# Kernel optimization log

Hardware: AMD Instinct MI355X
Metric: run time of the kernel (lower is better)

Reference implementation:

```python
import jax, jax.numpy as jnp
import numpy as np

NC = 2            # num_classes
CONF_THR = 0.7
IOU_THR = 0.2

_PI, _PJ = np.triu_indices(9, k=1)   # 36 candidate edge directions for min-area rect


def _decode_level(out, stride):
    # out: [C,h,w]; scale (x,y) channels by stride and add the pixel grid, flatten to [h*w, C]
    C, h, w = out.shape
    gw = (stride * jnp.arange(w, dtype=out.dtype))[None, :]
    gh = (stride * jnp.arange(h, dtype=out.dtype))[:, None]
    out = out.at[NC + 1].set(out[NC + 1] * stride + gw)
    out = out.at[NC + 2].set(out[NC + 2] * stride + gh)
    return out.reshape(C, -1).T


def _min_area_polygons(pts18):
    # pts18: (N,18) interleaved (a,b) coordinate pairs of 9 points.
    # Min-area enclosing rectangle: optimal rect is aligned with some point-pair direction;
    # brute-force all 36 pairs (superset of hull edges) -> exact result, fully vectorized.
    P = pts18.reshape(-1, 9, 2)                       # (N,9,2)
    d = P[:, _PJ] - P[:, _PI]                         # (N,36,2)
    nrm = jnp.sqrt(jnp.sum(d * d, -1) + 1e-12)
    c, s = d[..., 0] / nrm, d[..., 1] / nrm           # (N,36)
    a, b = P[..., 0][:, None, :], P[..., 1][:, None, :]   # (N,1,9)
    u = a * c[..., None] + b * s[..., None]           # rotate by -theta
    v = -a * s[..., None] + b * c[..., None]
    umin, umax = u.min(-1), u.max(-1)
    vmin, vmax = v.min(-1), v.max(-1)
    area = (umax - umin) * (vmax - vmin)              # (N,36)
    k = jnp.argmin(area, 1)[:, None]
    tk = lambda z: jnp.take_along_axis(z, k, 1)[:, 0]
    c, s, umin, umax, vmin, vmax = map(tk, (c, s, umin, umax, vmin, vmax))
    cu = jnp.stack([umin, umax, umax, umin], -1)      # rect corners in rotated frame
    cv = jnp.stack([vmin, vmin, vmax, vmax], -1)
    ca = cu * c[:, None] - cv * s[:, None]            # rotate back
    cb = cu * s[:, None] + cv * c[:, None]
    return jnp.stack([ca, cb], -1).reshape(-1, 8)     # (N,8) interleaved corners


def _points_in_quad(pts, quad):
    # pts (M,2), quad (4,2) convex with consistent winding -> (M,) bool
    e = jnp.roll(quad, -1, 0) - quad
    r = pts[:, None, :] - quad[None]
    cr = e[None, :, 0] * r[..., 1] - e[None, :, 1] * r[..., 0]
    return (cr >= 0).all(-1) | (cr <= 0).all(-1)


def _box_decoder(rect):
    # rect (N,8) -> (N,5) [cx, cy, w, h, angle]; y_first=True convention from the source
    w = jnp.sqrt((rect[:, 0] - rect[:, 2]) ** 2 + (rect[:, 1] - rect[:, 3]) ** 2)
    h = jnp.sqrt((rect[:, 4] - rect[:, 2]) ** 2 + (rect[:, 5] - rect[:, 3]) ** 2)
    cx = rect[:, 1:8:2].sum(1) * 0.25
    cy = rect[:, 0:8:2].sum(1) * 0.25
    ang = jnp.arctan((rect[:, 0] - rect[:, 2]) / (rect[:, 1] - rect[:, 3]))
    return jnp.stack([cx, cy, w, h, ang], -1)


def _rbox_corners(b):
    cx, cy, w, h, a = b[0], b[1], b[2], b[3], b[4]
    cs, sn = jnp.cos(a), jnp.sin(a)
    lx = jnp.array([-0.5, 0.5, 0.5, -0.5]) * w
    ly = jnp.array([-0.5, -0.5, 0.5, 0.5]) * h
    return jnp.stack([cx + lx * cs - ly * sn, cy + lx * sn + ly * cs], -1)  # (4,2)


def _quad_inter_area(A, B):
    # exact intersection area of two convex quads A,B (4,2):
    # candidates = corners of each inside the other + all 16 edge-edge intersections,
    # sorted by angle around their centroid, masked shoelace.
    inA = _points_in_quad(B, A)
    inB = _points_in_quad(A, B)
    rA = jnp.roll(A, -1, 0) - A
    rB = jnp.roll(B, -1, 0) - B
    qp = B[None] - A[:, None]                                  # (4,4,2)
    den = rA[:, None, 0] * rB[None, :, 1] - rA[:, None, 1] * rB[None, :, 0]
    dsafe = jnp.where(jnp.abs(den) < 1e-9, 1e-9, den)
    t = (qp[..., 0] * rB[None, :, 1] - qp[..., 1] * rB[None, :, 0]) / dsafe
    uu = (qp[..., 0] * rA[:, None, 1] - qp[..., 1] * rA[:, None, 0]) / dsafe
    okx = (jnp.abs(den) > 1e-9) & (t >= 0) & (t <= 1) & (uu >= 0) & (uu <= 1)
    X = A[:, None] + t[..., None] * rA[:, None]
    pts = jnp.concatenate([A, B, X.reshape(16, 2)], 0)          # (24,2)
    val = jnp.concatenate([inB, inA, okx.reshape(16)], 0)
    n = val.sum()
    cen = jnp.sum(jnp.where(val[:, None], pts, 0.0), 0) / jnp.maximum(n, 1)
    rel = pts - cen
    ang = jnp.where(val, jnp.arctan2(rel[:, 1], rel[:, 0]), 1e9)
    o = jnp.argsort(ang)
    rp, vs = rel[o], val[o]
    rp = jnp.where(vs[:, None], rp, rp[0])   # invalid slots -> first valid vertex (zero-area edges)
    nx = jnp.roll(rp, -1, 0)
    area = 0.5 * jnp.abs(jnp.sum(rp[:, 0] * nx[:, 1] - rp[:, 1] * nx[:, 0]))
    return jnp.where(n >= 3, area, 0.0)


def _forward(out3, out4, out5, off1_l3, off1_l4, off1_l5, offf_l3, offf_l4, offf_l5):
    outs = jnp.concatenate([_decode_level(out3[0], 4),
                            _decode_level(out4[0], 8),
                            _decode_level(out5[0], 16)], 0)          # (N, NC+3)
    flat = lambda z: z[0].reshape(18, -1).T
    off1 = jnp.concatenate([flat(off1_l3), flat(off1_l4), flat(off1_l5)], 0)
    offf = jnp.concatenate([flat(offf_l3), flat(offf_l4), flat(offf_l5)], 0) + off1
    N = outs.shape[0]
    x, y = outs[:, NC + 1], outs[:, NC + 2]
    offf = offf + jnp.tile(jnp.stack([y, x], -1), (1, 9))            # (y,x) interleaved, 9 points
    xs, ys = offf[:, 1:18:2], offf[:, 0:18:2]
    area = (xs.max(1) - xs.min(1)) * (ys.max(1) - ys.min(1)) / 40.0
    conf = outs[:, 0]
    conf_mask = conf > CONF_THR * jax.nn.sigmoid(area)
    rect = _min_area_polygons(offf)                                  # (N,8)
    boxes5 = _box_decoder(rect)                                      # (N,5)
    corners = jax.vmap(_rbox_corners)(boxes5)                        # (N,4,2)
    areas5 = boxes5[:, 2] * boxes5[:, 3]
    position = outs[:, NC + 1:]                                      # (N,2) = (x,y)
    pts_yx = jnp.stack([position[:, 1], position[:, 0]], -1)         # (y,x), matches rect plane
    quads = rect.reshape(N, 4, 2)
    order = jnp.argsort(jnp.where(conf_mask, conf, -jnp.inf))[::-1]

    def step(carry, i):
        suppressed, keep = carry
        active = jnp.logical_not(suppressed[i])
        keep = keep.at[i].set(active)
        inside = _points_in_quad(pts_yx, quads[i])                   # points_in_polygons
        inter = jax.vmap(lambda C: _quad_inter_area(corners[i], C))(corners)
        iou = inter / (areas5[i] + areas5 - inter + 1e-9)            # box_iou_rotated
        suppressed = suppressed | (active & (inside | (iou >= IOU_THR)))
        return (suppressed, keep), None

    init = (jnp.logical_not(conf_mask), jnp.zeros(N, dtype=bool))
    (_, keep), _ = jax.lax.scan(step, init, order)

    cls = outs[:, 1:NC + 1]
    maxc = cls.max(1)
    masks = jnp.stack([keep & (cls[:, i] == maxc) for i in range(NC)], 0)  # (NC,N)
    cnt = masks.sum(1)
    result = jnp.where(masks[:, :, None], position[None], 0.0)             # (NC,N,2) padded
    rect_out = rect * keep[:, None].astype(rect.dtype)                     # (N,8) padded
    return cnt, result, rect_out


def setup_inputs() -> dict:
    key = jax.random.key(0)
    shapes = [("out3", (1, NC + 3, 32, 32)), ("out4", (1, NC + 3, 16, 16)), ("out5", (1, NC + 3, 8, 8)),
              ("off1_l3", (1, 18, 32, 32)), ("off1_l4", (1, 18, 16, 16)), ("off1_l5", (1, 18, 8, 8)),
              ("offf_l3", (1, 18, 32, 32)), ("offf_l4", (1, 18, 16, 16)), ("offf_l5", (1, 18, 8, 8))]
    ks = jax.random.split(key, len(shapes))
    return {n: jax.random.normal(k, s, dtype=jnp.float32) for (n, s), k in zip(shapes, ks)}


def reference(out3, out4, out5, off1_l3, off1_l4, off1_l5, offf_l3, offf_l4, offf_l5):
    return _forward(out3, out4, out5, off1_l3, off1_l4, off1_l5, offf_l3, offf_l4, offf_l5)
```

## Files before the change

kernel.cpp:

```cpp
#include <hip/hip_runtime.h>
#include <math.h>

#define N_DET 1344
#define MW_MAX 8
#define T2S 9
#define QCAP 2048


__device__ __forceinline__ bool pt_in_quad4(const float* qx, const float* qy,
                                            float px, float py) {
    bool allp = true, alln = true;
#pragma unroll
    for (int k = 0; k < 4; k++) {
        int k1 = (k + 1) & 3;
        float ex = qx[k1] - qx[k], ey = qy[k1] - qy[k];
        float rx = px - qx[k],     ry = py - qy[k];
        float cr = ex * ry - ey * rx;
        allp = allp && (cr >= 0.f);
        alln = alln && (cr <= 0.f);
    }
    return allp || alln;
}

__device__ float quad_inter_area(const float* Ax, const float* Ay,
                                 const float* Bx, const float* By) {
    float px[24], py[24];
    unsigned vmask = 0;
    int n = 0;
#pragma unroll
    for (int k = 0; k < 4; k++) {
        px[k] = Ax[k]; py[k] = Ay[k];
        if (pt_in_quad4(Bx, By, Ax[k], Ay[k])) { vmask |= 1u << k; n++; }
    }
#pragma unroll
    for (int k = 0; k < 4; k++) {
        px[4 + k] = Bx[k]; py[4 + k] = By[k];
        if (pt_in_quad4(Ax, Ay, Bx[k], By[k])) { vmask |= 1u << (4 + k); n++; }
    }
#pragma unroll
    for (int k = 0; k < 4; k++) {
        int k1 = (k + 1) & 3;
        float rax = Ax[k1] - Ax[k], ray = Ay[k1] - Ay[k];
#pragma unroll
        for (int l = 0; l < 4; l++) {
            int l1 = (l + 1) & 3;
            float rbx = Bx[l1] - Bx[l], rby = By[l1] - By[l];
            float qpx = Bx[l] - Ax[k],  qpy = By[l] - Ay[k];
            float den = rax * rby - ray * rbx;
            float ad  = fabsf(den);
            float dsafe = (ad < 1e-9f) ? 1e-9f : den;
            float t = (qpx * rby - qpy * rbx) / dsafe;
            float u = (qpx * ray - qpy * rax) / dsafe;
            bool ok = (ad > 1e-9f) && t >= 0.f && t <= 1.f && u >= 0.f && u <= 1.f;
            int id = 8 + k * 4 + l;
            px[id] = Ax[k] + t * rax;
            py[id] = Ay[k] + t * ray;
            if (ok) { vmask |= 1u << id; n++; }
        }
    }
    float cx = 0.f, cy = 0.f;
#pragma unroll
    for (int m = 0; m < 24; m++)
        if ((vmask >> m) & 1u) { cx += px[m]; cy += py[m]; }
    int mx = (n < 1) ? 1 : n;
    cx = cx / (float)mx;
    cy = cy / (float)mx;

    unsigned long long key[32];
    float sx[32], sy[32];
#pragma unroll
    for (int m = 0; m < 24; m++) {
        float rx = px[m] - cx, ry = py[m] - cy;
        float a = ((vmask >> m) & 1u) ? atan2f(ry, rx) : 1e9f;
        unsigned u = __float_as_uint(a);
        u = (u & 0x80000000u) ? ~u : (u | 0x80000000u);
        key[m] = (((unsigned long long)u) << 6) | (unsigned)m;
        sx[m] = rx; sy[m] = ry;
    }
#pragma unroll
    for (int m = 24; m < 32; m++) { key[m] = ~0ull; sx[m] = 0.f; sy[m] = 0.f; }

#pragma unroll
    for (int k = 2; k <= 32; k <<= 1) {
#pragma unroll
        for (int j = k >> 1; j > 0; j >>= 1) {
#pragma unroll
            for (int t = 0; t < 32; t++) {
                int l = t ^ j;
                if (l > t) {
                    bool up = ((t & k) == 0);
                    bool sw = up ? (key[t] > key[l]) : (key[t] < key[l]);
                    if (sw) {
                        unsigned long long tk = key[t]; key[t] = key[l]; key[l] = tk;
                        float tx = sx[t]; sx[t] = sx[l]; sx[l] = tx;
                        float ty = sy[t]; sy[t] = sy[l]; sy[l] = ty;
                    }
                }
            }
        }
    }

    unsigned ut = __float_as_uint(1e9f) | 0x80000000u;
    unsigned long long kt = ((unsigned long long)ut) << 6;
    float fx = sx[0], fy = sy[0];
    float qx2[24], qy2[24];
#pragma unroll
    for (int m = 0; m < 24; m++) {
        bool v = key[m] < kt;
        qx2[m] = v ? sx[m] : fx;
        qy2[m] = v ? sy[m] : fy;
    }
    float ssum = 0.f;
#pragma unroll
    for (int m = 0; m < 24; m++) {
        int m1 = (m + 1) % 24;
        ssum += qx2[m] * qy2[m1] - qy2[m] * qx2[m1];
    }
    float area = 0.5f * fabsf(ssum);
    return (n >= 3) ? area : 0.f;
}

__device__ bool iou_suppress_c(const float* __restrict__ co_cor,
                               const float* __restrict__ co_a5, int p, int q) {
    float Axr[4], Ayr[4], Bxr[4], Byr[4];
#pragma unroll
    for (int k = 0; k < 4; k++) {
        Axr[k] = co_cor[p * 8 + 2 * k]; Ayr[k] = co_cor[p * 8 + 2 * k + 1];
        Bxr[k] = co_cor[q * 8 + 2 * k]; Byr[k] = co_cor[q * 8 + 2 * k + 1];
    }
    float inter = quad_inter_area(Axr, Ayr, Bxr, Byr);
    float iou = inter / (co_a5[p] + co_a5[q] - inter + 1e-9f);
    return iou >= 0.2f;
}

__global__ void k_decode(const float* __restrict__ out3, const float* __restrict__ out4,
                         const float* __restrict__ out5,
                         const float* __restrict__ o1l3, const float* __restrict__ o1l4,
                         const float* __restrict__ o1l5,
                         const float* __restrict__ ofl3, const float* __restrict__ ofl4,
                         const float* __restrict__ ofl5,
                         float* keyArr, float* cls0, float* cls1, float* xx, float* yy,
                         float* a5, float* ccx, float* ccy, float* rr,
                         float* rect, float* cor, int* Mcnt) {
    int n = blockIdx.x * blockDim.x + threadIdx.x;
    if (n >= N_DET) return;
    if (n == 0) *Mcnt = 0;
    const float *out, *o1, *of;
    int w, idx; float stride;
    if (n < 1024)      { out = out3; o1 = o1l3; of = ofl3; w = 32; idx = n;        stride = 4.f; }
    else if (n < 1280) { out = out4; o1 = o1l4; of = ofl4; w = 16; idx = n - 1024; stride = 8.f; }
    else               { out = out5; o1 = o1l5; of = ofl5; w = 8;  idx = n - 1280; stride = 16.f; }
    int hw = w * w;
    int row = idx / w, col = idx % w;
    float cf = out[0 * hw + idx];
    float c0 = out[1 * hw + idx];
    float c1 = out[2 * hw + idx];
    float x  = out[3 * hw + idx] * stride + stride * (float)col;
    float y  = out[4 * hw + idx] * stride + stride * (float)row;

    float Pa[9], Pb[9];
    float minb = INFINITY, maxb = -INFINITY, mina = INFINITY, maxa = -INFINITY;
#pragma unroll
    for (int k = 0; k < 9; k++) {
        float a = of[(2 * k) * hw + idx]     + o1[(2 * k) * hw + idx]     + y;
        float b = of[(2 * k + 1) * hw + idx] + o1[(2 * k + 1) * hw + idx] + x;
        Pa[k] = a; Pb[k] = b;
        mina = fminf(mina, a); maxa = fmaxf(maxa, a);
        minb = fminf(minb, b); maxb = fmaxf(maxb, b);
    }
    float area = (maxb - minb) * (maxa - mina) / 40.0f;
    float sg = 1.0f / (1.0f + expf(-area));
    int m = (cf > 0.7f * sg) ? 1 : 0;

    float best = INFINITY, bc = 0.f, bs = 0.f;
    float bumin = 0.f, bumax = 0.f, bvmin = 0.f, bvmax = 0.f;
#pragma unroll
    for (int i = 0; i < 9; i++) {
#pragma unroll
        for (int j = i + 1; j < 9; j++) {
            float d0 = Pa[j] - Pa[i], d1 = Pb[j] - Pb[i];
            float nr = sqrtf(d0 * d0 + d1 * d1 + 1e-12f);
            float c = d0 / nr, s = d1 / nr;
            float umin = INFINITY, umax = -INFINITY, vmin = INFINITY, vmax = -INFINITY;
#pragma unroll
            for (int k = 0; k < 9; k++) {
                float u =  Pa[k] * c + Pb[k] * s;
                float v = -Pa[k] * s + Pb[k] * c;
                umin = fminf(umin, u); umax = fmaxf(umax, u);
                vmin = fminf(vmin, v); vmax = fmaxf(vmax, v);
            }
            float ar = (umax - umin) * (vmax - vmin);
            if (ar < best) { best = ar; bc = c; bs = s;
                             bumin = umin; bumax = umax; bvmin = vmin; bvmax = vmax; }
        }
    }
    float cu[4] = {bumin, bumax, bumax, bumin};
    float cv[4] = {bvmin, bvmin, bvmax, bvmax};
    float r8[8];
#pragma unroll
    for (int k = 0; k < 4; k++) {
        r8[2 * k]     = cu[k] * bc - cv[k] * bs;
        r8[2 * k + 1] = cu[k] * bs + cv[k] * bc;
    }
    float w5 = sqrtf((r8[0] - r8[2]) * (r8[0] - r8[2]) + (r8[1] - r8[3]) * (r8[1] - r8[3]));
    float h5 = sqrtf((r8[4] - r8[2]) * (r8[4] - r8[2]) + (r8[5] - r8[3]) * (r8[5] - r8[3]));
    float cx = (r8[1] + r8[3] + r8[5] + r8[7]) * 0.25f;
    float cy = (r8[0] + r8[2] + r8[4] + r8[6]) * 0.25f;
    float ang = atanf((r8[0] - r8[2]) / (r8[1] - r8[3]));
    float cs = cosf(ang), sn = sinf(ang);
    const float lxs[4] = {-0.5f, 0.5f, 0.5f, -0.5f};
    const float lys[4] = {-0.5f, -0.5f, 0.5f, 0.5f};
#pragma unroll
    for (int k = 0; k < 4; k++) {
        cor[n * 8 + 2 * k]     = cx + lxs[k] * w5 * cs - lys[k] * h5 * sn;
        cor[n * 8 + 2 * k + 1] = cy + lxs[k] * w5 * sn + lys[k] * h5 * cs;
    }
#pragma unroll
    for (int k = 0; k < 8; k++) rect[n * 8 + k] = r8[k];
    keyArr[n] = m ? cf : -INFINITY;
    cls0[n] = c0; cls1[n] = c1;
    xx[n] = x; yy[n] = y; a5[n] = w5 * h5;
    ccx[n] = cx; ccy[n] = cy;
    rr[n] = 0.5f * sqrtf(w5 * w5 + h5 * h5);
}

__global__ __launch_bounds__(64) void k_order(
        const float* __restrict__ keyArr,
        const float* __restrict__ xx, const float* __restrict__ yy,
        const float* __restrict__ a5, const float* __restrict__ ccx,
        const float* __restrict__ ccy, const float* __restrict__ rr,
        const float* __restrict__ rect, const float* __restrict__ cor,
        int* order, int* Mcnt,
        float* co_ccx, float* co_ccy, float* co_rr, float* co_a5,
        float* co_xx, float* co_yy, float* co_rect, float* co_cor) {
    int b = blockIdx.x;
    int lane = threadIdx.x;
    float ki = keyArr[b];
    int rank = 0;
    for (int j = lane; j < N_DET; j += 64) {
        float kj = keyArr[j];
        rank += ((kj > ki) || (kj == ki && j > b)) ? 1 : 0;
    }
    for (int off = 32; off; off >>= 1) rank += __shfl_down(rank, off, 64);
    rank = __shfl(rank, 0, 64);
    if (lane == 0) {
        order[rank] = b;
        if (ki != -INFINITY) atomicAdd(Mcnt, 1);
    }
    if (lane < 8)            co_cor[rank * 8 + lane]        = cor[b * 8 + lane];
    else if (lane < 16)      co_rect[rank * 8 + (lane - 8)] = rect[b * 8 + (lane - 8)];
    else if (lane == 16)     co_ccx[rank] = ccx[b];
    else if (lane == 17)     co_ccy[rank] = ccy[b];
    else if (lane == 18)     co_rr[rank]  = rr[b];
    else if (lane == 19)     co_a5[rank]  = a5[b];
    else if (lane == 20)     co_xx[rank]  = xx[b];
    else if (lane == 21)     co_yy[rank]  = yy[b];
}

__global__ __launch_bounds__(256) void k_pairs(
        const float* __restrict__ co_rect, const float* __restrict__ co_cor,
        const float* __restrict__ co_a5,
        const float* __restrict__ co_xx, const float* __restrict__ co_yy,
        const float* __restrict__ co_ccx, const float* __restrict__ co_ccy,
        const float* __restrict__ co_rr,
        const int* __restrict__ Mcnt, unsigned long long* __restrict__ S2) {
    __shared__ unsigned int queue[QCAP];
    __shared__ int qn;
    int M = *Mcnt;
    int MW = (M + 63) >> 6;
    bool fast = (MW <= MW_MAX);
    int tid = threadIdx.x;
    int lane = tid & 63;
    if (tid == 0) qn = 0;
    __syncthreads();

    if (M > 0) {
        int gwave = (blockIdx.x * 256 + tid) >> 6;
        int nwave = (gridDim.x * 256) >> 6;
        int total = M * MW;
        for (int t = gwave; t < total; t += nwave) {
            int p = t / MW;
            int w = t - p * MW;
            int q = w * 64 + lane;
            bool valid = q < M;
            int qc = valid ? q : 0;

            float cbi = co_ccx[p], cai = co_ccy[p], ri = co_rr[p];
            float pjy = co_yy[qc], pjx = co_xx[qc];
            float da = pjy - cai, db = pjx - cbi;
            float rin = ri + 0.1f;
            bool inside = false;
            if (da * da + db * db <= rin * rin) {
                float qxr[4], qyr[4];
#pragma unroll
                for (int k = 0; k < 4; k++) { qxr[k] = co_rect[p * 8 + 2 * k]; qyr[k] = co_rect[p * 8 + 2 * k + 1]; }
                inside = pt_in_quad4(qxr, qyr, pjy, pjx);
            }
            bool bit = valid && inside;
            unsigned long long bb = __ballot(bit);

            float ex = cbi - co_ccx[qc], ey = cai - co_ccy[qc];
            float rs = ri + co_rr[qc] + 0.1f;
            bool needy = valid && (q != p) && !bit && (ex * ex + ey * ey <= rs * rs);

            if (fast) {
                if (lane == 0) S2[p * MW + w] = bb;
                unsigned long long pm = __ballot(needy);
                if (pm) {
                    int cw = __popcll(pm);
                    int base = 0;
                    if (lane == 0) base = atomicAdd(&qn, cw);
                    base = __shfl(base, 0, 64);
                    if (needy) {
                        int pos = base + __popcll(pm & ((1ull << lane) - 1ull));
                        if (pos < QCAP) {
                            queue[pos] = ((unsigned)p << 11) | (unsigned)q;
                        } else {
                            __threadfence();
                            if (iou_suppress_c(co_cor, co_a5, p, q))
                                atomicOr(&S2[p * MW + w], 1ull << (q & 63));
                        }
                    }
                }
            } else {
                bool supp = needy && iou_suppress_c(co_cor, co_a5, p, q);
                unsigned long long sb = __ballot(supp);
                if (lane == 0) S2[p * MW + w] = bb | sb;
            }
        }
    }
    __syncthreads();

    if (M > 0 && fast) {
        int cnt = qn; if (cnt > QCAP) cnt = QCAP;
        for (int t = tid; t < cnt; t += 256) {
            unsigned v = queue[t];
            int p = (int)(v >> 11), q = (int)(v & 2047u);
            if (iou_suppress_c(co_cor, co_a5, p, q))
                atomicOr(&S2[p * MW + (q >> 6)], 1ull << (q & 63));
        }
    }
}

__global__ __launch_bounds__(512) void k_scan_out(
    const float* __restrict__ cls0, const float* __restrict__ cls1,
    const float* __restrict__ xx, const float* __restrict__ yy,
    const float* __restrict__ rect,
    const int* __restrict__ order, const int* __restrict__ Mcnt,
    const unsigned long long* __restrict__ S2, float* __restrict__ out) {
    __shared__ unsigned long long T2[512 * T2S];
    __shared__ unsigned long long Kfin[MW_MAX];
    __shared__ unsigned int keep32[(N_DET + 31) / 32];
    __shared__ int cnt_s[2];
    int tid = threadIdx.x;
    int lane = tid & 63, wid = tid >> 6;
    int M = *Mcnt;
    int MW = (M + 63) >> 6;
    for (int t = tid; t < (N_DET + 31) / 32; t += 512) keep32[t] = 0u;
    if (tid < 2) cnt_s[tid] = 0;
    if (tid < MW_MAX) Kfin[tid] = 0ull;
    __syncthreads();

    if (M > 0 && MW <= MW_MAX) {
        for (int blk = wid; blk < MW * MW; blk += 8) {
            int wp = blk / MW, wq = blk - wp * MW;
            int pp = wp * 64 + lane;
            unsigned long long x = (pp < M) ? S2[pp * MW + wq] : 0ull;
#pragma unroll
            for (int b = 0; b < 64; b++) {
                unsigned long long bb = __ballot((x >> b) & 1ull);
                if (lane == b) T2[(wq * 64 + b) * T2S + wp] = bb;
            }
        }
        __syncthreads();

        if (wid == 0) {
            unsigned long long kw[MW_MAX];
#pragma unroll
            for (int w = 0; w < MW_MAX; w++) {
                int lo = w * 64;
                kw[w] = (M > lo) ? ((M - lo >= 64) ? ~0ull : ((1ull << (M - lo)) - 1ull)) : 0ull;
            }
            unsigned long long pmask = lane ? ((1ull << lane) - 1ull) : 0ull;
            for (int it = 0; it <= M; ++it) {
                bool changed = false;
#pragma unroll
                for (int k = 0; k < MW_MAX; k++) {
                    if (k < MW) {
                        int q = k * 64 + lane;
                        const unsigned long long* row = &T2[q * T2S];
                        unsigned long long sup = 0ull;
#pragma unroll
                        for (int w = 0; w < MW_MAX; w++) {
                            if (w < k)       sup |= row[w] & kw[w];
                            else if (w == k) sup |= row[w] & kw[w] & pmask;
                        }
                        bool nb = (q < M) && (sup == 0ull);
                        unsigned long long nw = __ballot(nb);
                        changed |= (nw != kw[k]);
                        kw[k] = nw;
                    }
                }
                if (!changed) break;
            }
            if (lane == 0) {
#pragma unroll
                for (int w = 0; w < MW_MAX; w++) Kfin[w] = kw[w];
            }
        }
        __syncthreads();
        for (int t = tid; t < M; t += 512) {
            if ((Kfin[t >> 6] >> (t & 63)) & 1ull) {
                int i = order[t];
                atomicOr(&keep32[i >> 5], 1u << (i & 31));
            }
        }
    } else if (M > 0) {
        if (wid == 0) {
            unsigned long long rem = 0ull;
            int lo = lane * 64;
            if (M > lo) rem = (M - lo >= 64) ? ~0ull : ((1ull << (M - lo)) - 1ull);
            for (int guard = 0; guard < N_DET; guard++) {
                unsigned long long vote = __ballot(rem != 0ull);
                if (!vote) break;
                int w = __builtin_ctzll(vote);
                unsigned long long wd = __shfl(rem, w, 64);
                int b = __builtin_ctzll(wd);
                int p = w * 64 + b;
                int i = order[p];
                if (lane == 0) atomicOr(&keep32[i >> 5], 1u << (i & 31));
                unsigned long long rowv = (lane < MW) ? S2[p * MW + lane] : 0ull;
                rem &= ~rowv;
                if (lane == w) rem &= ~(1ull << b);
            }
        }
    }
    __syncthreads();

    int c0 = 0, c1 = 0;
    for (int n = tid; n < N_DET; n += 512) {
        bool kp = (keep32[n >> 5] >> (n & 31)) & 1u;
        float a = cls0[n], b = cls1[n];
        float mxc = fmaxf(a, b);
        bool m0 = kp && (a == mxc);
        bool m1 = kp && (b == mxc);
        float x = xx[n], y = yy[n];
        out[2 + 0 * N_DET * 2 + n * 2 + 0] = m0 ? x : 0.f;
        out[2 + 0 * N_DET * 2 + n * 2 + 1] = m0 ? y : 0.f;
        out[2 + 1 * N_DET * 2 + n * 2 + 0] = m1 ? x : 0.f;
        out[2 + 1 * N_DET * 2 + n * 2 + 1] = m1 ? y : 0.f;
        float kf = kp ? 1.f : 0.f;
#pragma unroll
        for (int k = 0; k < 8; k++)
            out[2 + 2 * N_DET * 2 + n * 8 + k] = rect[n * 8 + k] * kf;
        c0 += m0 ? 1 : 0;
        c1 += m1 ? 1 : 0;
    }
    if (c0) atomicAdd(&cnt_s[0], c0);
    if (c1) atomicAdd(&cnt_s[1], c1);
    __syncthreads();
    if (tid == 0) { out[0] = (float)cnt_s[0]; out[1] = (float)cnt_s[1]; }
}

extern "C" void kernel_launch(void* const* d_in, const int* in_sizes, int n_in,
                              void* d_out, int out_size, void* d_ws, size_t ws_size,
                              hipStream_t stream) {
    const int N = N_DET;
    float* wsf = (float*)d_ws;

    const float* out3 = (const float*)d_in[0];
    const float* out4 = (const float*)d_in[1];
    const float* out5 = (const float*)d_in[2];
    const float* o1l3 = (const float*)d_in[3];
    const float* o1l4 = (const float*)d_in[4];
    const float* o1l5 = (const float*)d_in[5];
    const float* ofl3 = (const float*)d_in[6];
    const float* ofl4 = (const float*)d_in[7];
    const float* ofl5 = (const float*)d_in[8];
    float* out = (float*)d_out;

    float* keyArr = wsf + 0 * N;
    float* cls0   = wsf + 1 * N;
    float* cls1   = wsf + 2 * N;
    float* xx     = wsf + 3 * N;
    float* yy     = wsf + 4 * N;
    float* a5     = wsf + 5 * N;
    float* ccx    = wsf + 6 * N;
    float* ccy    = wsf + 7 * N;
    float* rr     = wsf + 8 * N;
    float* rect   = wsf + 9 * N;
    float* cor    = wsf + 17 * N;
    float* co_ccx = wsf + 25 * N;
    float* co_ccy = wsf + 26 * N;
    float* co_rr  = wsf + 27 * N;
    float* co_a5  = wsf + 28 * N;
    float* co_xx  = wsf + 29 * N;
    float* co_yy  = wsf + 30 * N;
    float* co_rect= wsf + 31 * N;
    float* co_cor = wsf + 39 * N;
    int* order    = (int*)(wsf + 47 * N);
    int* Mcnt     = order + N;
    unsigned long long* S2 = (unsigned long long*)(wsf + 48 * N + 8);

    k_decode<<<(N + 255) / 256, 256, 0, stream>>>(out3, out4, out5, o1l3, o1l4, o1l5,
                                                  ofl3, ofl4, ofl5,
                                                  keyArr, cls0, cls1, xx, yy, a5,
                                                  ccx, ccy, rr, rect, cor, Mcnt);
    k_order<<<N, 64, 0, stream>>>(keyArr, xx, yy, a5, ccx, ccy, rr, rect, cor,
                                  order, Mcnt,
                                  co_ccx, co_ccy, co_rr, co_a5, co_xx, co_yy,
                                  co_rect, co_cor);
    k_pairs<<<256, 256, 0, stream>>>(co_rect, co_cor, co_a5, co_xx, co_yy,
                                     co_ccx, co_ccy, co_rr, Mcnt, S2);
    k_scan_out<<<1, 512, 0, stream>>>(cls0, cls1, xx, yy, rect, order, Mcnt, S2, out);
}
```

Measured before the change: 127.8 us.

## Replace atomic valid-count with per-wave ballot counts and restructure NMS fixpoint

The global atomicAdd counter of valid detections is replaced by per-wavefront ballot popcounts written to 21 slots, which later kernels sum. k_order now packs four 64-lane wavefronts per 256-thread block instead of one block per detection. The keep-mask fixpoint in k_scan_out resolves each 64-bit word to convergence in order, instead of sweeping all words repeatedly until none change. This cuts atomic traffic and block count and shortens the serial greedy-NMS iteration, at the cost of extra small reads and a fixed 66-step guard per word.

After: 123.4 us (median of 2 runs). 3.4% less time.

```diff
diff --git a/kernel.cpp b/kernel.cpp
--- a/kernel.cpp
+++ b/kernel.cpp
@@ -133,6 +133,13 @@
     return iou >= 0.2f;
 }
 
+__device__ __forceinline__ int sum_mcount(const int* __restrict__ mcount_w) {
+    int M = 0;
+#pragma unroll
+    for (int k = 0; k < 21; k++) M += mcount_w[k];
+    return M;
+}
+
 __global__ void k_decode(const float* __restrict__ out3, const float* __restrict__ out4,
                          const float* __restrict__ out5,
                          const float* __restrict__ o1l3, const float* __restrict__ o1l4,
@@ -141,10 +148,9 @@
                          const float* __restrict__ ofl5,
                          float* keyArr, float* cls0, float* cls1, float* xx, float* yy,
                          float* a5, float* ccx, float* ccy, float* rr,
-                         float* rect, float* cor, int* Mcnt) {
+                         float* rect, float* cor, int* mcount_w) {
     int n = blockIdx.x * blockDim.x + threadIdx.x;
     if (n >= N_DET) return;
-    if (n == 0) *Mcnt = 0;
     const float *out, *o1, *of;
     int w, idx; float stride;
     if (n < 1024)      { out = out3; o1 = o1l3; of = ofl3; w = 32; idx = n;        stride = 4.f; }
@@ -222,19 +228,21 @@
     xx[n] = x; yy[n] = y; a5[n] = w5 * h5;
     ccx[n] = cx; ccy[n] = cy;
     rr[n] = 0.5f * sqrtf(w5 * w5 + h5 * h5);
-}
-
-__global__ __launch_bounds__(64) void k_order(
+    unsigned long long mb = __ballot(m != 0);
+    if ((threadIdx.x & 63) == 0) mcount_w[n >> 6] = (int)__popcll(mb);
+}
+
+__global__ __launch_bounds__(256) void k_order(
         const float* __restrict__ keyArr,
         const float* __restrict__ xx, const float* __restrict__ yy,
         const float* __restrict__ a5, const float* __restrict__ ccx,
         const float* __restrict__ ccy, const float* __restrict__ rr,
         const float* __restrict__ rect, const float* __restrict__ cor,
-        int* order, int* Mcnt,
+        int* order,
         float* co_ccx, float* co_ccy, float* co_rr, float* co_a5,
         float* co_xx, float* co_yy, float* co_rect, float* co_cor) {
-    int b = blockIdx.x;
-    int lane = threadIdx.x;
+    int lane = threadIdx.x & 63;
+    int b = blockIdx.x * 4 + (threadIdx.x >> 6);
     float ki = keyArr[b];
     int rank = 0;
     for (int j = lane; j < N_DET; j += 64) {
@@ -243,10 +251,7 @@
     }
     for (int off = 32; off; off >>= 1) rank += __shfl_down(rank, off, 64);
     rank = __shfl(rank, 0, 64);
-    if (lane == 0) {
-        order[rank] = b;
-        if (ki != -INFINITY) atomicAdd(Mcnt, 1);
-    }
+    if (lane == 0)           order[rank] = b;
     if (lane < 8)            co_cor[rank * 8 + lane]        = cor[b * 8 + lane];
     else if (lane < 16)      co_rect[rank * 8 + (lane - 8)] = rect[b * 8 + (lane - 8)];
     else if (lane == 16)     co_ccx[rank] = ccx[b];
@@ -263,10 +268,10 @@
         const float* __restrict__ co_xx, const float* __restrict__ co_yy,
         const float* __restrict__ co_ccx, const float* __restrict__ co_ccy,
         const float* __restrict__ co_rr,
-        const int* __restrict__ Mcnt, unsigned long long* __restrict__ S2) {
+        const int* __restrict__ mcount_w, unsigned long long* __restrict__ S2) {
     __shared__ unsigned int queue[QCAP];
     __shared__ int qn;
-    int M = *Mcnt;
+    int M = sum_mcount(mcount_w);
     int MW = (M + 63) >> 6;
     bool fast = (MW <= MW_MAX);
     int tid = threadIdx.x;
@@ -346,7 +351,7 @@
     const float* __restrict__ cls0, const float* __restrict__ cls1,
     const float* __restrict__ xx, const float* __restrict__ yy,
     const float* __restrict__ rect,
-    const int* __restrict__ order, const int* __restrict__ Mcnt,
+    const int* __restrict__ order, const int* __restrict__ mcount_w,
     const unsigned long long* __restrict__ S2, float* __restrict__ out) {
     __shared__ unsigned long long T2[512 * T2S];
     __shared__ unsigned long long Kfin[MW_MAX];
@@ -354,7 +359,7 @@
     __shared__ int cnt_s[2];
     int tid = threadIdx.x;
     int lane = tid & 63, wid = tid >> 6;
-    int M = *Mcnt;
+    int M = sum_mcount(mcount_w);
     int MW = (M + 63) >> 6;
     for (int t = tid; t < (N_DET + 31) / 32; t += 512) keep32[t] = 0u;
     if (tid < 2) cnt_s[tid] = 0;
@@ -376,36 +381,33 @@
 
         if (wid == 0) {
             unsigned long long kw[MW_MAX];
-#pragma unroll
-            for (int w = 0; w < MW_MAX; w++) {
-                int lo = w * 64;
-                kw[w] = (M > lo) ? ((M - lo >= 64) ? ~0ull : ((1ull << (M - lo)) - 1ull)) : 0ull;
-            }
             unsigned long long pmask = lane ? ((1ull << lane) - 1ull) : 0ull;
-            for (int it = 0; it <= M; ++it) {
-                bool changed = false;
-#pragma unroll
-                for (int k = 0; k < MW_MAX; k++) {
-                    if (k < MW) {
-                        int q = k * 64 + lane;
-                        const unsigned long long* row = &T2[q * T2S];
-                        unsigned long long sup = 0ull;
-#pragma unroll
-                        for (int w = 0; w < MW_MAX; w++) {
-                            if (w < k)       sup |= row[w] & kw[w];
-                            else if (w == k) sup |= row[w] & kw[w] & pmask;
-                        }
-                        bool nb = (q < M) && (sup == 0ull);
+#pragma unroll
+            for (int k = 0; k < MW_MAX; k++) {
+                if (k < MW) {
+                    int q = k * 64 + lane;
+                    const unsigned long long* row = &T2[q * T2S];
+                    unsigned long long base = 0ull;
+#pragma unroll
+                    for (int w = 0; w < MW_MAX; w++)
+                        if (w < k) base |= row[w] & kw[w];
+                    unsigned long long rk = row[k] & pmask;
+                    bool qv = q < M;
+                    int lo = k * 64;
+                    unsigned long long cur =
+                        (M - lo >= 64) ? ~0ull : ((1ull << (M - lo)) - 1ull);
+                    for (int guard = 0; guard < 66; guard++) {
+                        bool nb = qv && ((base | (rk & cur)) == 0ull);
                         unsigned long long nw = __ballot(nb);
-                        changed |= (nw != kw[k]);
-                        kw[k] = nw;
+                        if (nw == cur) break;
+                        cur = nw;
                     }
+                    kw[k] = cur;
                 }
-                if (!changed) break;
             }
             if (lane == 0) {
 #pragma unroll
-                for (int w = 0; w < MW_MAX; w++) Kfin[w] = kw[w];
+                for (int w = 0; w < MW_MAX; w++) Kfin[w] = (w < MW) ? kw[w] : 0ull;
             }
         }
         __syncthreads();
@@ -499,18 +501,18 @@
     float* co_rect= wsf + 31 * N;
     float* co_cor = wsf + 39 * N;
     int* order    = (int*)(wsf + 47 * N);
-    int* Mcnt     = order + N;
-    unsigned long long* S2 = (unsigned long long*)(wsf + 48 * N + 8);
+    int* mcount_w = order + N;
+    unsigned long long* S2 = (unsigned long long*)(wsf + 48 * N + 24);
 
     k_decode<<<(N + 255) / 256, 256, 0, stream>>>(out3, out4, out5, o1l3, o1l4, o1l5,
                                                   ofl3, ofl4, ofl5,
                                                   keyArr, cls0, cls1, xx, yy, a5,
-                                                  ccx, ccy, rr, rect, cor, Mcnt);
-    k_order<<<N, 64, 0, stream>>>(keyArr, xx, yy, a5, ccx, ccy, rr, rect, cor,
-                                  order, Mcnt,
-                                  co_ccx, co_ccy, co_rr, co_a5, co_xx, co_yy,
-                                  co_rect, co_cor);
+                                                  ccx, ccy, rr, rect, cor, mcount_w);
+    k_order<<<N / 4, 256, 0, stream>>>(keyArr, xx, yy, a5, ccx, ccy, rr, rect, cor,
+                                       order,
+                                       co_ccx, co_ccy, co_rr, co_a5, co_xx, co_yy,
+                                       co_rect, co_cor);
     k_pairs<<<256, 256, 0, stream>>>(co_rect, co_cor, co_a5, co_xx, co_yy,
-                                     co_ccx, co_ccy, co_rr, Mcnt, S2);
-    k_scan_out<<<1, 512, 0, stream>>>(cls0, cls1, xx, yy, rect, order, Mcnt, S2, out);
-}
+                                     co_ccx, co_ccy, co_rr, mcount_w, S2);
+    k_scan_out<<<1, 512, 0, stream>>>(cls0, cls1, xx, yy, rect, order, mcount_w, S2, out);
+}
```
